# Performance work log

Hardware: AMD Instinct MI355X
Metric: run time of the kernel (lower is better)

Reference implementation:

```python
import jax, jax.numpy as jnp
import numpy as np

N = 50000
E = 800000
IN_CH = 128
OUT_CH = 32
HEADS = 2
NEG_SLOPE = 0.2


def setup_inputs() -> dict:
    key = jax.random.key(0)
    k_x, k_ei, k_w, k_as, k_ad, k_b = jax.random.split(key, 6)
    x = jax.random.normal(k_x, (N, IN_CH), dtype=jnp.float32)
    edge_index = jax.random.randint(k_ei, (2, E), 0, N, dtype=jnp.int64)
    # Glorot-style init scale for linear weight and attention vectors
    w_scale = 1.0 / np.sqrt(IN_CH)
    W = jax.random.normal(k_w, (IN_CH, HEADS * OUT_CH), dtype=jnp.float32) * w_scale
    a_scale = 1.0 / np.sqrt(OUT_CH)
    a_src = jax.random.normal(k_as, (HEADS, OUT_CH), dtype=jnp.float32) * a_scale
    a_dst = jax.random.normal(k_ad, (HEADS, OUT_CH), dtype=jnp.float32) * a_scale
    bias = jnp.zeros((HEADS * OUT_CH,), dtype=jnp.float32)
    return {"x": x, "edge_index": edge_index, "W": W, "a_src": a_src,
            "a_dst": a_dst, "bias": bias}


def reference(x, edge_index, W, a_src, a_dst, bias):
    n = x.shape[0]
    # add self-loops (add_self_loops=True); static shape E+N
    loops = jnp.tile(jnp.arange(n, dtype=edge_index.dtype), (2, 1))
    ei = jnp.concatenate([edge_index, loops], axis=1)
    src, dst = ei[0], ei[1]

    # linear projection -> per-head features [N, H, C]
    h = (x @ W).reshape(n, HEADS, OUT_CH)

    # per-node attention logits [N, H]
    alpha_s = jnp.sum(h * a_src[None], axis=-1)
    alpha_d = jnp.sum(h * a_dst[None], axis=-1)

    # per-edge score, LeakyReLU, segment softmax over edges grouped by dst
    e = jax.nn.leaky_relu(alpha_s[src] + alpha_d[dst], NEG_SLOPE)  # [E', H]
    e_max = jax.ops.segment_max(e, dst, num_segments=n)           # [N, H]
    e_exp = jnp.exp(e - e_max[dst])
    denom = jax.ops.segment_sum(e_exp, dst, num_segments=n)       # [N, H]
    alpha = e_exp / (denom[dst] + 1e-16)                          # [E', H]

    # scatter-add weighted messages [N, H, C]
    out = jax.ops.segment_sum(alpha[:, :, None] * h[src], dst, num_segments=n)
    # concat heads + bias (concat=True)
    return out.reshape(n, HEADS * OUT_CH) + bias
```

## Files before the change

kernel.cpp:

```cpp
#include <hip/hip_runtime.h>
#include <hip/hip_bf16.h>
#include <hip/hip_fp16.h>
#include <math.h>

#define IN_CH   128
#define OUT_CH  32
#define HEADS   2
#define HC      (HEADS * OUT_CH)
#define NEG_SLOPE 0.2f

#define NODE_TILE 64
#define LDS_STRIDE 136

#define BIN_CAP 64

typedef _Float16 h2_t __attribute__((ext_vector_type(2)));
union V16 { int4 v; h2_t h[4]; };

__device__ __forceinline__ float fdot2(h2_t a, h2_t b, float c) {
#if __has_builtin(__builtin_amdgcn_fdot2)
    return __builtin_amdgcn_fdot2(a, b, c, false);
#else
    return c + (float)a.x * (float)b.x + (float)a.y * (float)b.y;
#endif
}

__global__ __launch_bounds__(256) void gemm_hist_kernel(
    const float* __restrict__ x, const float* __restrict__ W,
    const float* __restrict__ a_src, const float* __restrict__ a_dst,
    __half* __restrict__ h, float* __restrict__ alpha_s, float* __restrict__ alpha_d,
    const int* __restrict__ dst, int* __restrict__ deg, int* __restrict__ rank,
    int n_nodes, int n_edges, int n_total, int gemm_blocks)
{
    const int tid = threadIdx.x;

    if (blockIdx.x >= gemm_blocks) {
        int e = (blockIdx.x - gemm_blocks) * blockDim.x + tid;
        if (e < n_total) {
            int d = (e < n_edges) ? dst[e] : (e - n_edges);
            rank[e] = atomicAdd(&deg[d], 1);
        }
        return;
    }

    __shared__ _Float16 Wt[HC * LDS_STRIDE];
    __shared__ _Float16 Xs[NODE_TILE * LDS_STRIDE];

    const int node0 = blockIdx.x * NODE_TILE;

    const float4* W4 = (const float4*)W;
    #pragma unroll
    for (int i = 0; i < 8; ++i) {
        int idx4 = tid + i * 256;
        int k  = idx4 >> 4;
        int c4 = idx4 & 15;
        float4 v = W4[idx4];
        Wt[(c4 * 4 + 0) * LDS_STRIDE + k] = (_Float16)v.x;
        Wt[(c4 * 4 + 1) * LDS_STRIDE + k] = (_Float16)v.y;
        Wt[(c4 * 4 + 2) * LDS_STRIDE + k] = (_Float16)v.z;
        Wt[(c4 * 4 + 3) * LDS_STRIDE + k] = (_Float16)v.w;
    }

    const float4* X4 = (const float4*)x;
    #pragma unroll
    for (int i = 0; i < 8; ++i) {
        int idx4 = tid + i * 256;
        int r = idx4 >> 5, c4 = idx4 & 31;
        int node = node0 + r;
        float4 v = make_float4(0.f, 0.f, 0.f, 0.f);
        if (node < n_nodes) v = X4[(size_t)node * (IN_CH / 4) + c4];
        _Float16 hv[4] = {(_Float16)v.x, (_Float16)v.y, (_Float16)v.z, (_Float16)v.w};
        *(int2*)&Xs[r * LDS_STRIDE + c4 * 4] = *(int2*)hv;
    }
    __syncthreads();

    const int n    = tid >> 3;
    const int g    = tid & 7;
    const int col0 = g * 8;
    const int head = col0 >> 5;
    const int c0   = col0 & 31;

    float accA[8] = {0,0,0,0,0,0,0,0};
    float accB[8] = {0,0,0,0,0,0,0,0};
    const _Float16* xa = &Xs[n * LDS_STRIDE];
    const _Float16* xb = &Xs[(n + 32) * LDS_STRIDE];

    for (int k0 = 0; k0 < IN_CH; k0 += 8) {
        V16 va, vb;
        va.v = *(const int4*)&xa[k0];
        vb.v = *(const int4*)&xb[k0];
        #pragma unroll
        for (int j = 0; j < 8; ++j) {
            V16 w;
            w.v = *(const int4*)&Wt[(col0 + j) * LDS_STRIDE + k0];
            float a = accA[j], b = accB[j];
            a = fdot2(w.h[0], va.h[0], a); b = fdot2(w.h[0], vb.h[0], b);
            a = fdot2(w.h[1], va.h[1], a); b = fdot2(w.h[1], vb.h[1], b);
            a = fdot2(w.h[2], va.h[2], a); b = fdot2(w.h[2], vb.h[2], b);
            a = fdot2(w.h[3], va.h[3], a); b = fdot2(w.h[3], vb.h[3], b);
            accA[j] = a; accB[j] = b;
        }
    }

    float asr[8], adr[8];
    #pragma unroll
    for (int j = 0; j < 8; ++j) {
        asr[j] = a_src[head * OUT_CH + c0 + j];
        adr[j] = a_dst[head * OUT_CH + c0 + j];
    }

    #pragma unroll
    for (int half = 0; half < 2; ++half) {
        const float* acc = half ? accB : accA;
        const int node = node0 + n + half * 32;
        if (node < n_nodes) {
            unsigned u[8];
            #pragma unroll
            for (int j = 0; j < 8; ++j) u[j] = __half_as_ushort(__float2half_rn(acc[j]));
            int4 v = make_int4((int)(u[0] | (u[1] << 16)), (int)(u[2] | (u[3] << 16)),
                               (int)(u[4] | (u[5] << 16)), (int)(u[6] | (u[7] << 16)));
            *(int4*)&h[(size_t)node * HC + col0] = v;
        }
        float ps = 0.f, pd = 0.f;
        #pragma unroll
        for (int j = 0; j < 8; ++j) { ps += acc[j] * asr[j]; pd += acc[j] * adr[j]; }
        ps += __shfl_xor(ps, 1); ps += __shfl_xor(ps, 2);
        pd += __shfl_xor(pd, 1); pd += __shfl_xor(pd, 2);
        if ((g & 3) == 0 && node < n_nodes) {
            alpha_s[node * HEADS + head] = ps;
            alpha_d[node * HEADS + head] = pd;
        }
    }
}

__global__ void fill_kernel(const int* __restrict__ src, const int* __restrict__ dst,
                            const int* __restrict__ rank,
                            int* __restrict__ bins4, int n_edges, int n_total)
{
    int e = blockIdx.x * blockDim.x + threadIdx.x;
    if (e >= n_total) return;
    int s, d;
    if (e < n_edges) { s = src[e]; d = dst[e]; }
    else             { s = d = e - n_edges; }
    int rk = rank[e];
    if (rk < BIN_CAP) bins4[(size_t)d * BIN_CAP + rk] = s;
}

__global__ __launch_bounds__(256) void node_gather_kernel(
    const int* __restrict__ bins4, const int* __restrict__ deg,
    const float* __restrict__ alpha_s, const float* __restrict__ alpha_d,
    const __half* __restrict__ h, const float* __restrict__ bias,
    float* __restrict__ out, int n_nodes)
{
    __shared__ int2 stage[4][BIN_CAP];
    const int w = threadIdx.x >> 6;
    int node = blockIdx.x * 4 + w;
    if (node >= n_nodes) return;
    const int lane = threadIdx.x & 63;
    const int head = lane >> 5;
    int cnt = deg[node];
    if (cnt > BIN_CAP) cnt = BIN_CAP;

    float2 adn = ((const float2*)alpha_d)[node];

    int sreg = 0;
    float p0 = 0.f, p1 = 0.f;
    if (lane < cnt) {
        sreg = bins4[(size_t)node * BIN_CAP + lane];
        float2 a2 = ((const float2*)alpha_s)[sreg];
        float v0 = a2.x + adn.x;
        float v1 = a2.y + adn.y;
        v0 = (v0 > 0.f) ? v0 : NEG_SLOPE * v0;
        v1 = (v1 > 0.f) ? v1 : NEG_SLOPE * v1;
        p0 = __expf(v0);
        p1 = __expf(v1);
    }

    unsigned u0 = __half_as_ushort(__float2half_rn(p0));
    unsigned u1 = __half_as_ushort(__float2half_rn(p1));
    float q0 = __half2float(__ushort_as_half((unsigned short)u0));
    float q1 = __half2float(__ushort_as_half((unsigned short)u1));

    #pragma unroll
    for (int off = 1; off < 64; off <<= 1) {
        q0 += __shfl_xor(q0, off);
        q1 += __shfl_xor(q1, off);
    }
    const float lsum = head ? q1 : q0;

    stage[w][lane] = make_int2(sreg, (int)((u1 << 16) | u0));

    const unsigned hshift = (unsigned)head << 4;
    float acc = 0.f;
    for (int i = 0; i < cnt; i += 8) {
        #pragma unroll
        for (int j = 0; j < 8; ++j) {
            int2 rec = stage[w][i + j];
            float hj = __half2float(h[(size_t)rec.x * HC + lane]);
            float pj = __half2float(__ushort_as_half(
                           (unsigned short)(((unsigned)rec.y) >> hshift)));
            acc += pj * hj;
        }
    }
    out[(size_t)node * HC + lane] = acc / (lsum + 1e-16f) + bias[lane];
}

extern "C" void kernel_launch(void* const* d_in, const int* in_sizes, int n_in,
                              void* d_out, int out_size, void* d_ws, size_t ws_size,
                              hipStream_t stream)
{
    const float* x      = (const float*)d_in[0];
    const int*   ei     = (const int*)d_in[1];
    const float* W      = (const float*)d_in[2];
    const float* a_src  = (const float*)d_in[3];
    const float* a_dst  = (const float*)d_in[4];
    const float* bias   = (const float*)d_in[5];
    float* out = (float*)d_out;

    const int n_nodes = in_sizes[0] / IN_CH;
    const int n_edges = in_sizes[1] / 2;
    const int n_total = n_edges + n_nodes;

    const int* src = ei;
    const int* dst = ei + n_edges;

    __half* h      = (__half*)d_ws;
    float* alpha_s = (float*)(h + (size_t)n_nodes * HC);
    float* alpha_d = alpha_s + (size_t)n_nodes * HEADS;
    int* deg       = (int*)(alpha_d + (size_t)n_nodes * HEADS);
    int* rank      = deg + n_nodes;
    int* bins4     = rank + n_total;

    const int edge_blocks = (n_total + 255) / 256;
    const int gemm_blocks = (n_nodes + NODE_TILE - 1) / NODE_TILE;

    hipMemsetAsync(deg, 0, (size_t)n_nodes * sizeof(int), stream);

    gemm_hist_kernel<<<gemm_blocks + edge_blocks, 256, 0, stream>>>(
        x, W, a_src, a_dst, h, alpha_s, alpha_d,
        dst, deg, rank, n_nodes, n_edges, n_total, gemm_blocks);

    fill_kernel<<<edge_blocks, 256, 0, stream>>>(
        src, dst, rank, bins4, n_edges, n_total);

    int ng_blocks = (n_nodes + 3) / 4;
    node_gather_kernel<<<ng_blocks, 256, 0, stream>>>(
        bins4, deg, alpha_s, alpha_d, h, bias, out, n_nodes);
}
```

Measured before the change: 153.8 us.

## Fuse all stages into one persistent kernel with software grid barriers

Merges the GEMM/histogram, bin-fill and gather kernels into a single persistent kernel sized to occupancy times CU count. Stages are separated by atomic-counter grid barriers instead of kernel launches. This removes launch gaps and tail effects between kernels. In exchange it relies on all blocks being co-resident, adds spin-wait barrier cost, and uses grid-stride loops with fewer blocks, which may reduce latency hiding for the gather. The histogram atomics now run after the GEMM tiles rather than alongside them.

```diff
diff --git a/kernel.cpp b/kernel.cpp
--- a/kernel.cpp
+++ b/kernel.cpp
@@ -25,184 +25,193 @@
 #endif
 }
 
-__global__ __launch_bounds__(256) void gemm_hist_kernel(
+__device__ __forceinline__ void grid_barrier(int* ctr, int nblocks) {
+    __syncthreads();
+    if (threadIdx.x == 0) {
+        __threadfence();
+        __hip_atomic_fetch_add(ctr, 1, __ATOMIC_RELEASE, __HIP_MEMORY_SCOPE_AGENT);
+        while (__hip_atomic_load(ctr, __ATOMIC_ACQUIRE, __HIP_MEMORY_SCOPE_AGENT) < nblocks)
+            __builtin_amdgcn_s_sleep(4);
+        __threadfence();
+    }
+    __syncthreads();
+}
+
+__global__ __launch_bounds__(256, 4) void mega_kernel(
     const float* __restrict__ x, const float* __restrict__ W,
     const float* __restrict__ a_src, const float* __restrict__ a_dst,
+    const int* __restrict__ src, const int* __restrict__ dst,
     __half* __restrict__ h, float* __restrict__ alpha_s, float* __restrict__ alpha_d,
-    const int* __restrict__ dst, int* __restrict__ deg, int* __restrict__ rank,
-    int n_nodes, int n_edges, int n_total, int gemm_blocks)
+    int* __restrict__ deg, int* __restrict__ bar,
+    int* __restrict__ rank, int* __restrict__ bins4,
+    const float* __restrict__ bias, float* __restrict__ out,
+    int n_nodes, int n_edges, int n_total, int gemm_tiles, int nblocks)
 {
-    const int tid = threadIdx.x;
-
-    if (blockIdx.x >= gemm_blocks) {
-        int e = (blockIdx.x - gemm_blocks) * blockDim.x + tid;
-        if (e < n_total) {
-            int d = (e < n_edges) ? dst[e] : (e - n_edges);
-            rank[e] = atomicAdd(&deg[d], 1);
-        }
-        return;
-    }
-
     __shared__ _Float16 Wt[HC * LDS_STRIDE];
     __shared__ _Float16 Xs[NODE_TILE * LDS_STRIDE];
-
-    const int node0 = blockIdx.x * NODE_TILE;
-
-    const float4* W4 = (const float4*)W;
-    #pragma unroll
-    for (int i = 0; i < 8; ++i) {
-        int idx4 = tid + i * 256;
-        int k  = idx4 >> 4;
-        int c4 = idx4 & 15;
-        float4 v = W4[idx4];
-        Wt[(c4 * 4 + 0) * LDS_STRIDE + k] = (_Float16)v.x;
-        Wt[(c4 * 4 + 1) * LDS_STRIDE + k] = (_Float16)v.y;
-        Wt[(c4 * 4 + 2) * LDS_STRIDE + k] = (_Float16)v.z;
-        Wt[(c4 * 4 + 3) * LDS_STRIDE + k] = (_Float16)v.w;
-    }
-
-    const float4* X4 = (const float4*)x;
-    #pragma unroll
-    for (int i = 0; i < 8; ++i) {
-        int idx4 = tid + i * 256;
-        int r = idx4 >> 5, c4 = idx4 & 31;
-        int node = node0 + r;
-        float4 v = make_float4(0.f, 0.f, 0.f, 0.f);
-        if (node < n_nodes) v = X4[(size_t)node * (IN_CH / 4) + c4];
-        _Float16 hv[4] = {(_Float16)v.x, (_Float16)v.y, (_Float16)v.z, (_Float16)v.w};
-        *(int2*)&Xs[r * LDS_STRIDE + c4 * 4] = *(int2*)hv;
-    }
-    __syncthreads();
-
-    const int n    = tid >> 3;
-    const int g    = tid & 7;
-    const int col0 = g * 8;
-    const int head = col0 >> 5;
-    const int c0   = col0 & 31;
-
-    float accA[8] = {0,0,0,0,0,0,0,0};
-    float accB[8] = {0,0,0,0,0,0,0,0};
-    const _Float16* xa = &Xs[n * LDS_STRIDE];
-    const _Float16* xb = &Xs[(n + 32) * LDS_STRIDE];
-
-    for (int k0 = 0; k0 < IN_CH; k0 += 8) {
-        V16 va, vb;
-        va.v = *(const int4*)&xa[k0];
-        vb.v = *(const int4*)&xb[k0];
+    __shared__ int2 stage[4][BIN_CAP];
+
+    const int tid = threadIdx.x;
+    const int nb  = nblocks;
+
+    if ((int)blockIdx.x < gemm_tiles) {
+        const float4* W4 = (const float4*)W;
         #pragma unroll
-        for (int j = 0; j < 8; ++j) {
-            V16 w;
-            w.v = *(const int4*)&Wt[(col0 + j) * LDS_STRIDE + k0];
-            float a = accA[j], b = accB[j];
-            a = fdot2(w.h[0], va.h[0], a); b = fdot2(w.h[0], vb.h[0], b);
-            a = fdot2(w.h[1], va.h[1], a); b = fdot2(w.h[1], vb.h[1], b);
-            a = fdot2(w.h[2], va.h[2], a); b = fdot2(w.h[2], vb.h[2], b);
-            a = fdot2(w.h[3], va.h[3], a); b = fdot2(w.h[3], vb.h[3], b);
-            accA[j] = a; accB[j] = b;
-        }
-    }
-
-    float asr[8], adr[8];
-    #pragma unroll
-    for (int j = 0; j < 8; ++j) {
-        asr[j] = a_src[head * OUT_CH + c0 + j];
-        adr[j] = a_dst[head * OUT_CH + c0 + j];
-    }
-
-    #pragma unroll
-    for (int half = 0; half < 2; ++half) {
-        const float* acc = half ? accB : accA;
-        const int node = node0 + n + half * 32;
-        if (node < n_nodes) {
-            unsigned u[8];
-            #pragma unroll
-            for (int j = 0; j < 8; ++j) u[j] = __half_as_ushort(__float2half_rn(acc[j]));
-            int4 v = make_int4((int)(u[0] | (u[1] << 16)), (int)(u[2] | (u[3] << 16)),
-                               (int)(u[4] | (u[5] << 16)), (int)(u[6] | (u[7] << 16)));
-            *(int4*)&h[(size_t)node * HC + col0] = v;
-        }
-        float ps = 0.f, pd = 0.f;
+        for (int i = 0; i < 8; ++i) {
+            int idx4 = tid + i * 256;
+            int k  = idx4 >> 4;
+            int c4 = idx4 & 15;
+            float4 v = W4[idx4];
+            Wt[(c4 * 4 + 0) * LDS_STRIDE + k] = (_Float16)v.x;
+            Wt[(c4 * 4 + 1) * LDS_STRIDE + k] = (_Float16)v.y;
+            Wt[(c4 * 4 + 2) * LDS_STRIDE + k] = (_Float16)v.z;
+            Wt[(c4 * 4 + 3) * LDS_STRIDE + k] = (_Float16)v.w;
+        }
+
+        for (int t = blockIdx.x; t < gemm_tiles; t += nb) {
+            const int node0 = t * NODE_TILE;
+
+            const float4* X4 = (const float4*)x;
+            #pragma unroll
+            for (int i = 0; i < 8; ++i) {
+                int idx4 = tid + i * 256;
+                int r = idx4 >> 5, c4 = idx4 & 31;
+                int node = node0 + r;
+                float4 v = make_float4(0.f, 0.f, 0.f, 0.f);
+                if (node < n_nodes) v = X4[(size_t)node * (IN_CH / 4) + c4];
+                _Float16 hv[4] = {(_Float16)v.x, (_Float16)v.y, (_Float16)v.z, (_Float16)v.w};
+                *(int2*)&Xs[r * LDS_STRIDE + c4 * 4] = *(int2*)hv;
+            }
+            __syncthreads();
+
+            const int n    = tid >> 3;
+            const int g    = tid & 7;
+            const int col0 = g * 8;
+            const int head = col0 >> 5;
+            const int c0   = col0 & 31;
+
+            float accA[8] = {0,0,0,0,0,0,0,0};
+            float accB[8] = {0,0,0,0,0,0,0,0};
+            const _Float16* xa = &Xs[n * LDS_STRIDE];
+            const _Float16* xb = &Xs[(n + 32) * LDS_STRIDE];
+
+            for (int k0 = 0; k0 < IN_CH; k0 += 8) {
+                V16 va, vb;
+                va.v = *(const int4*)&xa[k0];
+                vb.v = *(const int4*)&xb[k0];
+                #pragma unroll
+                for (int j = 0; j < 8; ++j) {
+                    V16 w;
+                    w.v = *(const int4*)&Wt[(col0 + j) * LDS_STRIDE + k0];
+                    float a = accA[j], b = accB[j];
+                    a = fdot2(w.h[0], va.h[0], a); b = fdot2(w.h[0], vb.h[0], b);
+                    a = fdot2(w.h[1], va.h[1], a); b = fdot2(w.h[1], vb.h[1], b);
+                    a = fdot2(w.h[2], va.h[2], a); b = fdot2(w.h[2], vb.h[2], b);
+                    a = fdot2(w.h[3], va.h[3], a); b = fdot2(w.h[3], vb.h[3], b);
+                    accA[j] = a; accB[j] = b;
+                }
+            }
+
+            float asr[8], adr[8];
+            #pragma unroll
+            for (int j = 0; j < 8; ++j) {
+                asr[j] = a_src[head * OUT_CH + c0 + j];
+                adr[j] = a_dst[head * OUT_CH + c0 + j];
+            }
+
+            #pragma unroll
+            for (int half = 0; half < 2; ++half) {
+                const float* acc = half ? accB : accA;
+                const int node = node0 + n + half * 32;
+                if (node < n_nodes) {
+                    unsigned u[8];
+                    #pragma unroll
+                    for (int j = 0; j < 8; ++j) u[j] = __half_as_ushort(__float2half_rn(acc[j]));
+                    int4 v = make_int4((int)(u[0] | (u[1] << 16)), (int)(u[2] | (u[3] << 16)),
+                                       (int)(u[4] | (u[5] << 16)), (int)(u[6] | (u[7] << 16)));
+                    *(int4*)&h[(size_t)node * HC + col0] = v;
+                }
+                float ps = 0.f, pd = 0.f;
+                #pragma unroll
+                for (int j = 0; j < 8; ++j) { ps += acc[j] * asr[j]; pd += acc[j] * adr[j]; }
+                ps += __shfl_xor(ps, 1); ps += __shfl_xor(ps, 2);
+                pd += __shfl_xor(pd, 1); pd += __shfl_xor(pd, 2);
+                if ((g & 3) == 0 && node < n_nodes) {
+                    alpha_s[node * HEADS + head] = ps;
+                    alpha_d[node * HEADS + head] = pd;
+                }
+            }
+            __syncthreads();
+        }
+    }
+
+    for (int e = blockIdx.x * 256 + tid; e < n_total; e += nb * 256) {
+        int d = (e < n_edges) ? dst[e] : (e - n_edges);
+        rank[e] = atomicAdd(&deg[d], 1);
+    }
+
+    grid_barrier(&bar[0], nb);
+
+    for (int e = blockIdx.x * 256 + tid; e < n_total; e += nb * 256) {
+        int s, d;
+        if (e < n_edges) { s = src[e]; d = dst[e]; }
+        else             { s = d = e - n_edges; }
+        int rk = rank[e];
+        if (rk < BIN_CAP) bins4[(size_t)d * BIN_CAP + rk] = s;
+    }
+
+    grid_barrier(&bar[1], nb);
+
+    const int w    = tid >> 6;
+    const int lane = tid & 63;
+    const int head = lane >> 5;
+    for (int node = blockIdx.x * 4 + w; node < n_nodes; node += nb * 4) {
+        int cnt = deg[node];
+        if (cnt > BIN_CAP) cnt = BIN_CAP;
+
+        float2 adn = ((const float2*)alpha_d)[node];
+
+        int sreg = 0;
+        float p0 = 0.f, p1 = 0.f;
+        if (lane < cnt) {
+            sreg = bins4[(size_t)node * BIN_CAP + lane];
+            float2 a2 = ((const float2*)alpha_s)[sreg];
+            float v0 = a2.x + adn.x;
+            float v1 = a2.y + adn.y;
+            v0 = (v0 > 0.f) ? v0 : NEG_SLOPE * v0;
+            v1 = (v1 > 0.f) ? v1 : NEG_SLOPE * v1;
+            p0 = __expf(v0);
+            p1 = __expf(v1);
+        }
+
+        unsigned u0 = __half_as_ushort(__float2half_rn(p0));
+        unsigned u1 = __half_as_ushort(__float2half_rn(p1));
+        float q0 = __half2float(__ushort_as_half((unsigned short)u0));
+        float q1 = __half2float(__ushort_as_half((unsigned short)u1));
+
         #pragma unroll
-        for (int j = 0; j < 8; ++j) { ps += acc[j] * asr[j]; pd += acc[j] * adr[j]; }
-        ps += __shfl_xor(ps, 1); ps += __shfl_xor(ps, 2);
-        pd += __shfl_xor(pd, 1); pd += __shfl_xor(pd, 2);
-        if ((g & 3) == 0 && node < n_nodes) {
-            alpha_s[node * HEADS + head] = ps;
-            alpha_d[node * HEADS + head] = pd;
-        }
-    }
-}
-
-__global__ void fill_kernel(const int* __restrict__ src, const int* __restrict__ dst,
-                            const int* __restrict__ rank,
-                            int* __restrict__ bins4, int n_edges, int n_total)
-{
-    int e = blockIdx.x * blockDim.x + threadIdx.x;
-    if (e >= n_total) return;
-    int s, d;
-    if (e < n_edges) { s = src[e]; d = dst[e]; }
-    else             { s = d = e - n_edges; }
-    int rk = rank[e];
-    if (rk < BIN_CAP) bins4[(size_t)d * BIN_CAP + rk] = s;
-}
-
-__global__ __launch_bounds__(256) void node_gather_kernel(
-    const int* __restrict__ bins4, const int* __restrict__ deg,
-    const float* __restrict__ alpha_s, const float* __restrict__ alpha_d,
-    const __half* __restrict__ h, const float* __restrict__ bias,
-    float* __restrict__ out, int n_nodes)
-{
-    __shared__ int2 stage[4][BIN_CAP];
-    const int w = threadIdx.x >> 6;
-    int node = blockIdx.x * 4 + w;
-    if (node >= n_nodes) return;
-    const int lane = threadIdx.x & 63;
-    const int head = lane >> 5;
-    int cnt = deg[node];
-    if (cnt > BIN_CAP) cnt = BIN_CAP;
-
-    float2 adn = ((const float2*)alpha_d)[node];
-
-    int sreg = 0;
-    float p0 = 0.f, p1 = 0.f;
-    if (lane < cnt) {
-        sreg = bins4[(size_t)node * BIN_CAP + lane];
-        float2 a2 = ((const float2*)alpha_s)[sreg];
-        float v0 = a2.x + adn.x;
-        float v1 = a2.y + adn.y;
-        v0 = (v0 > 0.f) ? v0 : NEG_SLOPE * v0;
-        v1 = (v1 > 0.f) ? v1 : NEG_SLOPE * v1;
-        p0 = __expf(v0);
-        p1 = __expf(v1);
-    }
-
-    unsigned u0 = __half_as_ushort(__float2half_rn(p0));
-    unsigned u1 = __half_as_ushort(__float2half_rn(p1));
-    float q0 = __half2float(__ushort_as_half((unsigned short)u0));
-    float q1 = __half2float(__ushort_as_half((unsigned short)u1));
-
-    #pragma unroll
-    for (int off = 1; off < 64; off <<= 1) {
-        q0 += __shfl_xor(q0, off);
-        q1 += __shfl_xor(q1, off);
-    }
-    const float lsum = head ? q1 : q0;
-
-    stage[w][lane] = make_int2(sreg, (int)((u1 << 16) | u0));
-
-    const unsigned hshift = (unsigned)head << 4;
-    float acc = 0.f;
-    for (int i = 0; i < cnt; i += 8) {
-        #pragma unroll
-        for (int j = 0; j < 8; ++j) {
-            int2 rec = stage[w][i + j];
-            float hj = __half2float(h[(size_t)rec.x * HC + lane]);
-            float pj = __half2float(__ushort_as_half(
-                           (unsigned short)(((unsigned)rec.y) >> hshift)));
-            acc += pj * hj;
-        }
-    }
-    out[(size_t)node * HC + lane] = acc / (lsum + 1e-16f) + bias[lane];
+        for (int off = 1; off < 64; off <<= 1) {
+            q0 += __shfl_xor(q0, off);
+            q1 += __shfl_xor(q1, off);
+        }
+        const float lsum = head ? q1 : q0;
+
+        stage[w][lane] = make_int2(sreg, (int)((u1 << 16) | u0));
+
+        const unsigned hshift = (unsigned)head << 4;
+        float acc = 0.f;
+        for (int i = 0; i < cnt; i += 8) {
+            #pragma unroll
+            for (int j = 0; j < 8; ++j) {
+                int2 rec = stage[w][i + j];
+                float hj = __half2float(h[(size_t)rec.x * HC + lane]);
+                float pj = __half2float(__ushort_as_half(
+                               (unsigned short)(((unsigned)rec.y) >> hshift)));
+                acc += pj * hj;
+            }
+        }
+        out[(size_t)node * HC + lane] = acc / (lsum + 1e-16f) + bias[lane];
+    }
 }
 
 extern "C" void kernel_launch(void* const* d_in, const int* in_sizes, int n_in,
@@ -228,22 +237,27 @@
     float* alpha_s = (float*)(h + (size_t)n_nodes * HC);
     float* alpha_d = alpha_s + (size_t)n_nodes * HEADS;
     int* deg       = (int*)(alpha_d + (size_t)n_nodes * HEADS);
-    int* rank      = deg + n_nodes;
+    int* bar       = deg + n_nodes;
+    int* rank      = bar + 2;
     int* bins4     = rank + n_total;
 
-    const int edge_blocks = (n_total + 255) / 256;
-    const int gemm_blocks = (n_nodes + NODE_TILE - 1) / NODE_TILE;
-
-    hipMemsetAsync(deg, 0, (size_t)n_nodes * sizeof(int), stream);
-
-    gemm_hist_kernel<<<gemm_blocks + edge_blocks, 256, 0, stream>>>(
-        x, W, a_src, a_dst, h, alpha_s, alpha_d,
-        dst, deg, rank, n_nodes, n_edges, n_total, gemm_blocks);
-
-    fill_kernel<<<edge_blocks, 256, 0, stream>>>(
-        src, dst, rank, bins4, n_edges, n_total);
-
-    int ng_blocks = (n_nodes + 3) / 4;
-    node_gather_kernel<<<ng_blocks, 256, 0, stream>>>(
-        bins4, deg, alpha_s, alpha_d, h, bias, out, n_nodes);
-}
+    const int gemm_tiles = (n_nodes + NODE_TILE - 1) / NODE_TILE;
+
+    int occ = 0;
+    (void)hipOccupancyMaxActiveBlocksPerMultiprocessor(&occ, mega_kernel, 256, 0);
+    if (occ < 1) occ = 2;
+    if (occ > 4) occ = 4;
+    int numCU = 0;
+    int dev = 0;
+    (void)hipGetDevice(&dev);
+    (void)hipDeviceGetAttribute(&numCU, hipDeviceAttributeMultiprocessorCount, dev);
+    if (numCU <= 0) numCU = 256;
+    const int nb = occ * numCU;
+
+    hipMemsetAsync(deg, 0, (size_t)(n_nodes + 2) * sizeof(int), stream);
+
+    mega_kernel<<<nb, 256, 0, stream>>>(
+        x, W, a_src, a_dst, src, dst,
+        h, alpha_s, alpha_d, deg, bar, rank, bins4,
+        bias, out, n_nodes, n_edges, n_total, gemm_tiles, nb);
+}
```

Result: slower. 366.7 us (+138.4%).

## Vectorize gather loads per lane and pair GEMM with bin fill instead of histogram

Applied to the files above, without the earlier changes.

The node gather now has each lane load 4 contiguous half channels (8 bytes) for a quarter of the edge group, then sums the partial results across lane quarters with shuffles. This replaces many scalar 2-byte loads with fewer wider ones and adds independent accumulators for more memory-level parallelism. The launch order also changes: the atomic histogram runs as its own kernel, and the GEMM is fused with the bin-fill pass instead. The costs are extra shuffle reductions and only a quarter of the lanes doing the final store.

```diff
diff --git a/kernel.cpp b/kernel.cpp
--- a/kernel.cpp
+++ b/kernel.cpp
@@ -25,11 +25,21 @@
 #endif
 }
 
-__global__ __launch_bounds__(256) void gemm_hist_kernel(
+__global__ void hist_kernel(const int* __restrict__ dst, int* __restrict__ deg,
+                            int* __restrict__ rank, int n_edges, int n_total)
+{
+    int e = blockIdx.x * blockDim.x + threadIdx.x;
+    if (e >= n_total) return;
+    int d = (e < n_edges) ? dst[e] : (e - n_edges);
+    rank[e] = atomicAdd(&deg[d], 1);
+}
+
+__global__ __launch_bounds__(256) void gemm_fill_kernel(
     const float* __restrict__ x, const float* __restrict__ W,
     const float* __restrict__ a_src, const float* __restrict__ a_dst,
     __half* __restrict__ h, float* __restrict__ alpha_s, float* __restrict__ alpha_d,
-    const int* __restrict__ dst, int* __restrict__ deg, int* __restrict__ rank,
+    const int* __restrict__ src, const int* __restrict__ dst,
+    const int* __restrict__ rank, int* __restrict__ bins4,
     int n_nodes, int n_edges, int n_total, int gemm_blocks)
 {
     const int tid = threadIdx.x;
@@ -37,8 +47,11 @@
     if (blockIdx.x >= gemm_blocks) {
         int e = (blockIdx.x - gemm_blocks) * blockDim.x + tid;
         if (e < n_total) {
-            int d = (e < n_edges) ? dst[e] : (e - n_edges);
-            rank[e] = atomicAdd(&deg[d], 1);
+            int s, d;
+            if (e < n_edges) { s = src[e]; d = dst[e]; }
+            else             { s = d = e - n_edges; }
+            int rk = rank[e];
+            if (rk < BIN_CAP) bins4[(size_t)d * BIN_CAP + rk] = s;
         }
         return;
     }
@@ -133,19 +146,6 @@
     }
 }
 
-__global__ void fill_kernel(const int* __restrict__ src, const int* __restrict__ dst,
-                            const int* __restrict__ rank,
-                            int* __restrict__ bins4, int n_edges, int n_total)
-{
-    int e = blockIdx.x * blockDim.x + threadIdx.x;
-    if (e >= n_total) return;
-    int s, d;
-    if (e < n_edges) { s = src[e]; d = dst[e]; }
-    else             { s = d = e - n_edges; }
-    int rk = rank[e];
-    if (rk < BIN_CAP) bins4[(size_t)d * BIN_CAP + rk] = s;
-}
-
 __global__ __launch_bounds__(256) void node_gather_kernel(
     const int* __restrict__ bins4, const int* __restrict__ deg,
     const float* __restrict__ alpha_s, const float* __restrict__ alpha_d,
@@ -157,7 +157,6 @@
     int node = blockIdx.x * 4 + w;
     if (node >= n_nodes) return;
     const int lane = threadIdx.x & 63;
-    const int head = lane >> 5;
     int cnt = deg[node];
     if (cnt > BIN_CAP) cnt = BIN_CAP;
 
@@ -186,23 +185,48 @@
         q0 += __shfl_xor(q0, off);
         q1 += __shfl_xor(q1, off);
     }
+
+    stage[w][lane] = make_int2(sreg, (int)((u1 << 16) | u0));
+
+    const int q    = lane >> 4;
+    const int c0   = (lane & 15) * 4;
+    const int head = c0 >> 5;
+    const unsigned hshift = (unsigned)head << 4;
     const float lsum = head ? q1 : q0;
 
-    stage[w][lane] = make_int2(sreg, (int)((u1 << 16) | u0));
-
-    const unsigned hshift = (unsigned)head << 4;
-    float acc = 0.f;
+    float acc0 = 0.f, acc1 = 0.f, acc2 = 0.f, acc3 = 0.f;
     for (int i = 0; i < cnt; i += 8) {
-        #pragma unroll
-        for (int j = 0; j < 8; ++j) {
-            int2 rec = stage[w][i + j];
-            float hj = __half2float(h[(size_t)rec.x * HC + lane]);
-            float pj = __half2float(__ushort_as_half(
-                           (unsigned short)(((unsigned)rec.y) >> hshift)));
-            acc += pj * hj;
-        }
-    }
-    out[(size_t)node * HC + lane] = acc / (lsum + 1e-16f) + bias[lane];
+        int2 recA = stage[w][i + q];
+        int2 recB = stage[w][i + 4 + q];
+        int2 hvA = *(const int2*)&h[(size_t)recA.x * HC + c0];
+        int2 hvB = *(const int2*)&h[(size_t)recB.x * HC + c0];
+        float pA = __half2float(__ushort_as_half(
+                       (unsigned short)(((unsigned)recA.y) >> hshift)));
+        float pB = __half2float(__ushort_as_half(
+                       (unsigned short)(((unsigned)recB.y) >> hshift)));
+        float2 fA01 = __half22float2(*(const __half2*)&hvA.x);
+        float2 fA23 = __half22float2(*(const __half2*)&hvA.y);
+        float2 fB01 = __half22float2(*(const __half2*)&hvB.x);
+        float2 fB23 = __half22float2(*(const __half2*)&hvB.y);
+        acc0 += pA * fA01.x + pB * fB01.x;
+        acc1 += pA * fA01.y + pB * fB01.y;
+        acc2 += pA * fA23.x + pB * fB23.x;
+        acc3 += pA * fA23.y + pB * fB23.y;
+    }
+
+    acc0 += __shfl_xor(acc0, 16); acc0 += __shfl_xor(acc0, 32);
+    acc1 += __shfl_xor(acc1, 16); acc1 += __shfl_xor(acc1, 32);
+    acc2 += __shfl_xor(acc2, 16); acc2 += __shfl_xor(acc2, 32);
+    acc3 += __shfl_xor(acc3, 16); acc3 += __shfl_xor(acc3, 32);
+
+    if (q == 0) {
+        float inv = 1.f / (lsum + 1e-16f);
+        const float4* b4 = (const float4*)bias;
+        float4 bv = b4[c0 >> 2];
+        float4 o = make_float4(acc0 * inv + bv.x, acc1 * inv + bv.y,
+                               acc2 * inv + bv.z, acc3 * inv + bv.w);
+        *(float4*)&out[(size_t)node * HC + c0] = o;
+    }
 }
 
 extern "C" void kernel_launch(void* const* d_in, const int* in_sizes, int n_in,
@@ -236,12 +260,11 @@
 
     hipMemsetAsync(deg, 0, (size_t)n_nodes * sizeof(int), stream);
 
-    gemm_hist_kernel<<<gemm_blocks + edge_blocks, 256, 0, stream>>>(
+    hist_kernel<<<edge_blocks, 256, 0, stream>>>(dst, deg, rank, n_edges, n_total);
+
+    gemm_fill_kernel<<<gemm_blocks + edge_blocks, 256, 0, stream>>>(
         x, W, a_src, a_dst, h, alpha_s, alpha_d,
-        dst, deg, rank, n_nodes, n_edges, n_total, gemm_blocks);
-
-    fill_kernel<<<edge_blocks, 256, 0, stream>>>(
-        src, dst, rank, bins4, n_edges, n_total);
+        src, dst, rank, bins4, n_nodes, n_edges, n_total, gemm_blocks);
 
     int ng_blocks = (n_nodes + 3) / 4;
     node_gather_kernel<<<ng_blocks, 256, 0, stream>>>(
```

Result: slower. 174.0 us (+13.1%).
